# Performance work log

Hardware: AMD Instinct MI355X
Metric: run time of the kernel (lower is better)

## Reference

```python
import jax, jax.numpy as jnp
import numpy as np

B = 256
N_VERTS = 10475
N_JOINTS = 55  # 1 root + 21 body + jaw + 2 eyes + 2*15 hands
NUM_BETAS = 10
NUM_EXPR = 10
POSE_BASIS = (N_JOINTS - 1) * 9  # 486
# SMPL-X kinematic tree (parent index per joint, root = -1)
PARENTS = np.array([-1,0,0,0,1,2,3,4,5,6,7,8,9,9,9,12,13,14,16,17,18,19,15,15,15,
                    20,25,26,20,28,29,20,31,32,20,34,35,20,37,38,
                    21,40,41,21,43,44,21,46,47,21,49,50,21,52,53], dtype=np.int64)


def _rodrigues(aa):
    # axis-angle [..., 3] -> rotation matrix [..., 3, 3]
    angle = jnp.linalg.norm(aa, axis=-1, keepdims=True) + 1e-8
    axis = aa / angle
    x, y, z = axis[..., 0], axis[..., 1], axis[..., 2]
    zero = jnp.zeros_like(x)
    K = jnp.stack([zero, -z, y, z, zero, -x, -y, x, zero], axis=-1).reshape(aa.shape[:-1] + (3, 3))
    s = jnp.sin(angle)[..., None]
    c = jnp.cos(angle)[..., None]
    I = jnp.eye(3, dtype=aa.dtype)
    return I + s * K + (1.0 - c) * (K @ K)


def setup_inputs() -> dict:
    key = jax.random.key(0)
    ks = jax.random.split(key, 16)
    def rots(k, nj, scale=0.2):
        aa = jax.random.normal(k, (B, nj, 3), dtype=jnp.float32) * scale
        return _rodrigues(aa)
    inp = {
        'world_rot': rots(ks[0], 1, 0.5),
        'world_tsl': jax.random.normal(ks[1], (B, 3), dtype=jnp.float32),
        'body_shape': jax.random.normal(ks[2], (B, NUM_BETAS), dtype=jnp.float32),
        'body_pose': rots(ks[3], 21),
        'left_hand_pose': rots(ks[4], 15),
        'right_hand_pose': rots(ks[5], 15),
        'expr_shape': jax.random.normal(ks[6], (B, NUM_EXPR), dtype=jnp.float32),
        'jaw_pose': rots(ks[7], 1),
        'leye_pose': rots(ks[8], 1),
        'reye_pose': rots(ks[9], 1),
        # model buffers (synthetic, SMPL-X-sized)
        'v_template': jax.random.normal(ks[10], (N_VERTS, 3), dtype=jnp.float32) * 0.3,
        'shapedirs': jax.random.normal(ks[11], (N_VERTS, 3, NUM_BETAS), dtype=jnp.float32) * 0.01,
        'expr_dirs': jax.random.normal(ks[12], (N_VERTS, 3, NUM_EXPR), dtype=jnp.float32) * 0.01,
        'posedirs': jax.random.normal(ks[13], (POSE_BASIS, N_VERTS * 3), dtype=jnp.float32) * 0.01,
        'J_regressor': jax.nn.softmax(jax.random.normal(ks[14], (N_JOINTS, N_VERTS), dtype=jnp.float32) * 4.0, axis=-1),
        'lbs_weights': jax.nn.softmax(jax.random.normal(ks[15], (N_VERTS, N_JOINTS), dtype=jnp.float32) * 4.0, axis=-1),
    }
    return inp


def _lbs(world_rot, world_tsl, body_shape, body_pose, left_hand_pose, right_hand_pose,
         expr_shape, jaw_pose, leye_pose, reye_pose,
         v_template, shapedirs, expr_dirs, posedirs, J_regressor, lbs_weights):
    dtype = v_template.dtype
    # full pose: [B, 55, 3, 3]
    full_pose = jnp.concatenate([world_rot, body_pose, jaw_pose, leye_pose, reye_pose,
                                 left_hand_pose, right_hand_pose], axis=1)
    b = full_pose.shape[0]
    # shape + expression blendshapes
    v_shaped = v_template[None] + jnp.einsum('bk,nck->bnc', body_shape, shapedirs) \
               + jnp.einsum('bk,nck->bnc', expr_shape, expr_dirs)
    # rest-pose joints [B, J, 3]
    joints = jnp.einsum('jn,bnc->bjc', J_regressor, v_shaped)
    # pose blendshapes
    ident = jnp.eye(3, dtype=dtype)
    pose_feature = (full_pose[:, 1:] - ident).reshape(b, POSE_BASIS)
    v_posed = v_shaped + (pose_feature @ posedirs).reshape(b, N_VERTS, 3)
    # relative joint locations w.r.t. parent
    rel_joints = joints.at[:, 1:].add(-joints[:, PARENTS[1:]])
    # local 4x4 transforms [B, J, 4, 4]
    top = jnp.concatenate([full_pose, rel_joints[..., None]], axis=-1)  # [B,J,3,4]
    bottom = jnp.broadcast_to(jnp.array([0., 0., 0., 1.], dtype=dtype), (b, N_JOINTS, 1, 4))
    T = jnp.concatenate([top, bottom], axis=2)
    # kinematic chain recurrence (small fixed joint count -> unrolled)
    chain = [T[:, 0]]
    for i in range(1, N_JOINTS):
        chain.append(chain[PARENTS[i]] @ T[:, i])
    A = jnp.stack(chain, axis=1)  # [B, J, 4, 4]
    posed_joints = A[..., :3, 3]
    # remove rest-pose joint offset so A maps rest -> posed
    t_corr = posed_joints - jnp.einsum('bjkl,bjl->bjk', A[..., :3, :3], joints)
    A_rel = A.at[..., :3, 3].set(t_corr)
    # linear blend skinning: per-vertex transform [B, N, 4, 4]
    T_vert = jnp.einsum('nj,bjkl->bnkl', lbs_weights, A_rel)
    verts = jnp.einsum('bnkl,bnl->bnk', T_vert[..., :3, :3], v_posed) + T_vert[..., :3, 3]
    verts = verts + world_tsl[:, None]
    joints_out = posed_joints + world_tsl[:, None]
    return verts, joints_out


def reference(world_rot, world_tsl, body_shape, body_pose, left_hand_pose, right_hand_pose,
              expr_shape, jaw_pose, leye_pose, reye_pose,
              v_template, shapedirs, expr_dirs, posedirs, J_regressor, lbs_weights):
    return _lbs(world_rot, world_tsl, body_shape, body_pose, left_hand_pose, right_hand_pose,
                expr_shape, jaw_pose, leye_pose, reye_pose,
                v_template, shapedirs, expr_dirs, posedirs, J_regressor, lbs_weights)
```

## Files before the change

### kernel.cpp

```cpp
#include <hip/hip_runtime.h>
#include <stdint.h>

#define BATCH 256
#define NV 10475
#define NVP 10496
#define NJ 55
#define PB 486
#define KS 506
#define VC (NV*3)
#define KP 512
#define BKC 32
#define NCHUNK 16
#define BN 64
#define JCH 8
#define JCHUNK 1312

typedef short bf16x8 __attribute__((ext_vector_type(8)));
typedef float f32x4  __attribute__((ext_vector_type(4)));

__constant__ int c_parents[NJ] = {
  -1,0,0,0,1,2,3,4,5,6,7,8,9,9,9,12,13,14,16,17,18,19,15,15,15,
  20,25,26,20,28,29,20,31,32,20,34,35,20,37,38,21,40,41,21,43,44,
  21,46,47,21,49,50,21,52,53};

__constant__ int c_depth[NJ] = {
  0,1,1,1,2,2,2,3,3,3,4,4,4,4,4,5,5,5,6,6,7,7,6,6,6,
  8,9,10,8,9,10,8,9,10,8,9,10,8,9,10,
  8,9,10,8,9,10,8,9,10,8,9,10,8,9,10};

__device__ __forceinline__ unsigned short f2bf(float x){
  uint32_t u = __float_as_uint(x);
  uint32_t r = (u + 0x7fffu + ((u >> 16) & 1u)) >> 16;
  return (unsigned short)r;
}
__device__ __forceinline__ float bf2f(unsigned short h){
  return __uint_as_float(((uint32_t)h) << 16);
}

__global__ __launch_bounds__(256) void k_prep(
    const float* __restrict__ lw, unsigned short* __restrict__ lwb) {
  int idx = blockIdx.x*256 + threadIdx.x;
  int n = idx >> 6, j = idx & 63;
  float v = (n < NV && j < NJ) ? lw[(size_t)n*NJ + j] : 0.f;
  unsigned short hi = f2bf(v);
  float lo = v - bf2f(hi);
  lwb[idx] = hi;
  lwb[(size_t)NVP*64 + idx] = f2bf(lo);
}

__device__ __forceinline__ const float* pose_src(int j, int b,
    const float* wrot, const float* bpose, const float* jaw, const float* leye,
    const float* reye, const float* lhand, const float* rhand) {
  if (j==0)  return wrot  + b*9;
  if (j<=21) return bpose + (b*21 + (j-1))*9;
  if (j==22) return jaw   + b*9;
  if (j==23) return leye  + b*9;
  if (j==24) return reye  + b*9;
  if (j<=39) return lhand + (b*15 + (j-25))*9;
  return rhand + (b*15 + (j-40))*9;
}

__global__ __launch_bounds__(512) void k_posefeat(
    const float* __restrict__ bpose, const float* __restrict__ jaw,
    const float* __restrict__ leye, const float* __restrict__ reye,
    const float* __restrict__ lhand, const float* __restrict__ rhand,
    const float* __restrict__ bs, const float* __restrict__ es,
    unsigned short* __restrict__ pfb) {
  int b = blockIdx.x, t = threadIdx.x;
  unsigned short o = 0;
  if (t < PB){
    int jj = t/9, rc = t - jj*9;
    const float* rs = pose_src(jj+1, b, nullptr, bpose, jaw, leye, reye, lhand, rhand);
    float v = rs[rc];
    if (rc==0 || rc==4 || rc==8) v -= 1.0f;
    o = f2bf(v);
  } else if (t < 496){
    o = f2bf(bs[b*10 + (t-486)]);
  } else if (t < KS){
    o = f2bf(es[b*10 + (t-496)]);
  }
  pfb[(size_t)b*KP + t] = o;
}

__global__ __launch_bounds__(256) void k_jsmall(
    const float* __restrict__ jreg, const float* __restrict__ sd,
    const float* __restrict__ ed, const float* __restrict__ vt,
    float* __restrict__ part) {
  int ch = blockIdx.x, j = blockIdx.y;
  int t = threadIdx.x;
  float acc[63];
  #pragma unroll
  for (int s=0;s<63;s++) acc[s]=0.f;
  int n0 = ch*JCHUNK, nend = min(n0+JCHUNK, NV);
  for (int n = n0 + t; n < nend; n += 256){
    float w = jreg[(size_t)j*NV + n];
    const float* sp = sd + (size_t)n*30;
    const float* ep = ed + (size_t)n*30;
    const float* vp = vt + (size_t)n*3;
    #pragma unroll
    for (int c=0;c<3;c++){
      #pragma unroll
      for (int q=0;q<10;q++){
        acc[c*21+q]    += w*sp[c*10+q];
        acc[c*21+10+q] += w*ep[c*10+q];
      }
      acc[c*21+20] += w*vp[c];
    }
  }
  #pragma unroll
  for (int s=0;s<63;s++){
    float a = acc[s];
    #pragma unroll
    for (int d=32; d>=1; d>>=1) a += __shfl_xor(a,d);
    acc[s]=a;
  }
  __shared__ float red[4][63];
  int w = t>>6, l = t&63;
  if (l==0){
    #pragma unroll
    for (int s=0;s<63;s++) red[w][s]=acc[s];
  }
  __syncthreads();
  if (t < 63){
    float a = red[0][t]+red[1][t]+red[2][t]+red[3][t];
    part[((size_t)j*JCH+ch)*63 + t] = a;
  }
}

__global__ __launch_bounds__(192) void k_joints2(
    const float* __restrict__ part, const float* __restrict__ bs,
    const float* __restrict__ es, float* __restrict__ joints) {
  int b = blockIdx.x, t = threadIdx.x;
  if (t >= NJ*3) return;
  int j = t/3, c = t - j*3;
  float S[21];
  #pragma unroll
  for (int q=0;q<21;q++) S[q]=0.f;
  for (int ch=0; ch<JCH; ch++){
    const float* p = part + ((size_t)j*JCH+ch)*63 + c*21;
    #pragma unroll
    for (int q=0;q<21;q++) S[q] += p[q];
  }
  float a = S[20];
  #pragma unroll
  for (int q=0;q<10;q++) a += S[q]*bs[b*10+q] + S[10+q]*es[b*10+q];
  joints[(size_t)b*NJ*3 + t] = a;
}

__global__ __launch_bounds__(256) void k_chain(
    const float* __restrict__ wrot, const float* __restrict__ bpose,
    const float* __restrict__ jaw, const float* __restrict__ leye,
    const float* __restrict__ reye, const float* __restrict__ lhand,
    const float* __restrict__ rhand, const float* __restrict__ wtsl,
    const float* __restrict__ joints,
    unsigned short* __restrict__ arelb, float* __restrict__ jout) {
  const int w = threadIdx.x >> 6, lane = threadIdx.x & 63;
  const int b = blockIdx.x*4 + w;
  const int j = lane;
  const bool act = (j < NJ);

  float R[9] = {1.f,0.f,0.f, 0.f,1.f,0.f, 0.f,0.f,1.f};
  if (act){
    const float* rs = pose_src(j, b, wrot, bpose, jaw, leye, reye, lhand, rhand);
    #pragma unroll
    for (int i=0;i<9;i++) R[i]=rs[i];
  }
  float jx=0.f, jy=0.f, jz=0.f;
  if (act){
    const float* jb = joints + (size_t)b*NJ*3 + j*3;
    jx=jb[0]; jy=jb[1]; jz=jb[2];
  }
  int par = act ? c_parents[j] : 0;
  if (par < 0) par = 0;
  float px = __shfl(jx, par), py = __shfl(jy, par), pz = __shfl(jz, par);
  float t0, t1, t2;
  if (j == 0){ t0=jx; t1=jy; t2=jz; }
  else       { t0=jx-px; t1=jy-py; t2=jz-pz; }

  float M[12];
  #pragma unroll
  for (int r=0;r<3;r++){
    M[r*4+0]=R[r*3+0]; M[r*4+1]=R[r*3+1]; M[r*4+2]=R[r*3+2]; M[r*4+3]= (r==0?t0:(r==1?t1:t2));
  }
  int dep = act ? c_depth[j] : 99;

  #pragma unroll
  for (int L=1; L<=10; L++){
    float pm[12];
    #pragma unroll
    for (int i=0;i<12;i++) pm[i] = __shfl(M[i], par);
    if (dep == L){
      #pragma unroll
      for (int r=0;r<3;r++){
        float p0=pm[r*4+0], p1=pm[r*4+1], p2=pm[r*4+2], p3=pm[r*4+3];
        M[r*4+0] = p0*R[0]+p1*R[3]+p2*R[6];
        M[r*4+1] = p0*R[1]+p1*R[4]+p2*R[7];
        M[r*4+2] = p0*R[2]+p1*R[5]+p2*R[8];
        M[r*4+3] = p0*t0 + p1*t1 + p2*t2 + p3;
      }
    }
  }

  float wx=wtsl[b*3+0], wy=wtsl[b*3+1], wz=wtsl[b*3+2];
  if (act){
    jout[((size_t)b*NJ+j)*3+0] = M[3]  + wx;
    jout[((size_t)b*NJ+j)*3+1] = M[7]  + wy;
    jout[((size_t)b*NJ+j)*3+2] = M[11] + wz;
  }
  float A[12];
  #pragma unroll
  for (int r=0;r<3;r++){
    A[r*4+0]=M[r*4+0]; A[r*4+1]=M[r*4+1]; A[r*4+2]=M[r*4+2];
    A[r*4+3]=M[r*4+3] - (M[r*4+0]*jx + M[r*4+1]*jy + M[r*4+2]*jz);
  }
  unsigned short* ah = arelb + (size_t)(b*2+0)*16*64;
  unsigned short* al = arelb + (size_t)(b*2+1)*16*64;
  #pragma unroll
  for (int e=0;e<16;e++){
    float v = (e < 12 && act) ? A[e] : 0.f;
    unsigned short hi = f2bf(v);
    float lo = v - bf2f(hi);
    ah[e*64 + j] = hi;
    al[e*64 + j] = f2bf(lo);
  }
}

__global__ __launch_bounds__(256, 2) void k_vposed(
    const float* __restrict__ pd, const float* __restrict__ sd,
    const float* __restrict__ ed, const float* __restrict__ vt,
    const unsigned short* __restrict__ pfb, float* __restrict__ vsh) {
  const int tid  = threadIdx.x;
  const int w    = tid >> 6, lane = tid & 63;
  const int m16  = lane & 15, quad = lane >> 4;
  const int col0 = blockIdx.x * BN;

  f32x4 acc[4][4];
  #pragma unroll
  for (int i=0;i<4;i++)
    #pragma unroll
    for (int j=0;j<4;j++) acc[i][j] = (f32x4){0.f,0.f,0.f,0.f};

  int bcol[4];
  #pragma unroll
  for (int ni=0;ni<4;ni++) bcol[ni] = min(col0 + ni*16 + m16, VC-1);

  const unsigned short* pfa = pfb + (size_t)(w*64 + m16)*KP + quad*8;

  #pragma unroll 2
  for (int c=0; c<15; c++){
    const int k0 = c*BKC;
    bf16x8 a[4];
    #pragma unroll
    for (int mi=0;mi<4;mi++)
      a[mi] = *((const bf16x8*)(pfa + (size_t)mi*16*KP + k0));
    union { bf16x8 v; unsigned short s[8]; } bb[4];
    #pragma unroll
    for (int ni=0;ni<4;ni++){
      #pragma unroll
      for (int j=0;j<8;j++){
        int kk = k0 + quad*8 + j;
        bb[ni].s[j] = f2bf(pd[(size_t)kk*VC + bcol[ni]]);
      }
    }
    #pragma unroll
    for (int mi=0;mi<4;mi++)
      #pragma unroll
      for (int ni=0;ni<4;ni++)
        acc[mi][ni] = __builtin_amdgcn_mfma_f32_16x16x32_bf16(
                          a[mi], bb[ni].v, acc[mi][ni], 0, 0, 0);
  }
  {
    const int k0 = 15*BKC;
    bf16x8 a[4];
    #pragma unroll
    for (int mi=0;mi<4;mi++)
      a[mi] = *((const bf16x8*)(pfa + (size_t)mi*16*KP + k0));
    union { bf16x8 v; unsigned short s[8]; } bb[4];
    #pragma unroll
    for (int ni=0;ni<4;ni++){
      int n3 = bcol[ni]/3, c3 = bcol[ni] - n3*3;
      const float* sp = sd + (size_t)n3*30 + c3*10;
      const float* ep = ed + (size_t)n3*30 + c3*10;
      #pragma unroll
      for (int j=0;j<8;j++){
        int kk = k0 + quad*8 + j;
        float f = 0.f;
        if (kk < PB)      f = pd[(size_t)kk*VC + bcol[ni]];
        else if (kk < KS){
          int q = kk - PB;
          f = (q < 10) ? sp[q] : ep[q-10];
        }
        bb[ni].s[j] = f2bf(f);
      }
    }
    #pragma unroll
    for (int mi=0;mi<4;mi++)
      #pragma unroll
      for (int ni=0;ni<4;ni++)
        acc[mi][ni] = __builtin_amdgcn_mfma_f32_16x16x32_bf16(
                          a[mi], bb[ni].v, acc[mi][ni], 0, 0, 0);
  }
  #pragma unroll
  for (int mi=0;mi<4;mi++){
    int rbase = w*64 + mi*16 + quad*4;
    #pragma unroll
    for (int ni=0;ni<4;ni++){
      int col = col0 + ni*16 + m16;
      if (col < VC){
        float vtc = vt[col];
        #pragma unroll
        for (int r=0;r<4;r++)
          vsh[(size_t)(rbase + r)*VC + col] = acc[mi][ni][r] + vtc;
      }
    }
  }
}

__global__ __launch_bounds__(256) void k_verts(
    const unsigned short* __restrict__ lwb, const unsigned short* __restrict__ arelb,
    const float* __restrict__ wtsl, float* __restrict__ out) {
  __shared__ float sT[4*64*17];
  const int tid = threadIdx.x, w = tid >> 6, lane = tid & 63;
  const int m16 = lane & 15, quad = lane >> 4;
  const int n0 = blockIdx.x*64;
  const int b0 = blockIdx.y*16;
  float* myT = &sT[w*64*17];

  bf16x8 lwh[4][2], lwl[4][2];
  #pragma unroll
  for (int vt4=0; vt4<4; vt4++){
    int row = n0 + vt4*16 + m16;
    #pragma unroll
    for (int kc=0;kc<2;kc++){
      lwh[vt4][kc] = *((const bf16x8*)(lwb + (size_t)row*64 + kc*32 + quad*8));
      lwl[vt4][kc] = *((const bf16x8*)(lwb + (size_t)NVP*64 + (size_t)row*64 + kc*32 + quad*8));
    }
  }
  const int nA = n0 + lane;
  const bool okA = (nA < NV);

  for (int bi=0; bi<4; bi++){
    const int b = b0 + w*4 + bi;
    bf16x8 ah[2], al[2];
    #pragma unroll
    for (int kc=0;kc<2;kc++){
      ah[kc] = *((const bf16x8*)(arelb + ((size_t)(b*2+0)*16 + m16)*64 + kc*32 + quad*8));
      al[kc] = *((const bf16x8*)(arelb + ((size_t)(b*2+1)*16 + m16)*64 + kc*32 + quad*8));
    }
    const float* vp = out + ((size_t)b*NV + nA)*3;
    float vx = okA ? vp[0] : 0.f;
    float vy = okA ? vp[1] : 0.f;
    float vz = okA ? vp[2] : 0.f;

    f32x4 acc[4];
    #pragma unroll
    for (int vt4=0; vt4<4; vt4++) acc[vt4] = (f32x4){0.f,0.f,0.f,0.f};
    #pragma unroll
    for (int vt4=0; vt4<4; vt4++){
      #pragma unroll
      for (int kc=0;kc<2;kc++){
        acc[vt4] = __builtin_amdgcn_mfma_f32_16x16x32_bf16(ah[kc], lwh[vt4][kc], acc[vt4], 0,0,0);
        acc[vt4] = __builtin_amdgcn_mfma_f32_16x16x32_bf16(al[kc], lwh[vt4][kc], acc[vt4], 0,0,0);
        acc[vt4] = __builtin_amdgcn_mfma_f32_16x16x32_bf16(ah[kc], lwl[vt4][kc], acc[vt4], 0,0,0);
      }
    }
    #pragma unroll
    for (int vt4=0; vt4<4; vt4++){
      #pragma unroll
      for (int r=0;r<4;r++)
        myT[(vt4*16 + m16)*17 + quad*4 + r] = acc[vt4][r];
    }
    float T[12];
    const float* Tp = &myT[lane*17];
    #pragma unroll
    for (int e=0;e<12;e++) T[e] = Tp[e];
    if (okA){
      float tx=wtsl[b*3+0], ty=wtsl[b*3+1], tz=wtsl[b*3+2];
      float* op = out + ((size_t)b*NV + nA)*3;
      op[0] = T[0]*vx + T[1]*vy + T[2] *vz + T[3]  + tx;
      op[1] = T[4]*vx + T[5]*vy + T[6] *vz + T[7]  + ty;
      op[2] = T[8]*vx + T[9]*vy + T[10]*vz + T[11] + tz;
    }
  }
}

extern "C" void kernel_launch(void* const* d_in, const int* in_sizes, int n_in,
                              void* d_out, int out_size, void* d_ws, size_t ws_size,
                              hipStream_t stream) {
  const float* wrot   = (const float*)d_in[0];
  const float* wtsl   = (const float*)d_in[1];
  const float* bshape = (const float*)d_in[2];
  const float* bpose  = (const float*)d_in[3];
  const float* lhand  = (const float*)d_in[4];
  const float* rhand  = (const float*)d_in[5];
  const float* eshape = (const float*)d_in[6];
  const float* jaw    = (const float*)d_in[7];
  const float* leye   = (const float*)d_in[8];
  const float* reye   = (const float*)d_in[9];
  const float* vt     = (const float*)d_in[10];
  const float* sd     = (const float*)d_in[11];
  const float* ed     = (const float*)d_in[12];
  const float* pd     = (const float*)d_in[13];
  const float* jreg   = (const float*)d_in[14];
  const float* lw     = (const float*)d_in[15];
  float* out = (float*)d_out;

  float* vsh  = out;
  float* jout = out + (size_t)BATCH*NV*3;

  float* ws     = (float*)d_ws;
  float* joints = ws;
  float* part   = joints + (size_t)BATCH*NJ*3;
  unsigned short* pfb   = (unsigned short*)(part + (size_t)NJ*JCH*63);
  unsigned short* lwb   = pfb + (size_t)BATCH*KP;
  unsigned short* arelb = lwb + (size_t)2*NVP*64;

  const int PREP_BLOCKS = (NVP*64)/256;

  k_prep    <<<PREP_BLOCKS, 256, 0, stream>>>(lw, lwb);
  k_posefeat<<<BATCH, 512, 0, stream>>>(bpose, jaw, leye, reye, lhand, rhand,
                                        bshape, eshape, pfb);
  k_jsmall  <<<dim3(JCH, NJ), 256, 0, stream>>>(jreg, sd, ed, vt, part);
  k_joints2 <<<BATCH, 192, 0, stream>>>(part, bshape, eshape, joints);
  k_chain   <<<64, 256, 0, stream>>>(wrot, bpose, jaw, leye, reye, lhand, rhand,
                                     wtsl, joints, arelb, jout);
  k_vposed  <<<(VC+BN-1)/BN, 256, 0, stream>>>(pd, sd, ed, vt, pfb, vsh);
  k_verts   <<<dim3(NVP/64, 16), 256, 0, stream>>>(lwb, arelb, wtsl, out);
}
```

Measured before the change: 246.9 us.

## Pre-pack posedirs to bf16 MFMA layout and widen vposed blocks

Adds a prep stage that converts posedirs plus the shape and expression dirs into a padded bf16 buffer laid out in MFMA B-fragment order. The vposed GEMM then does one vector load per fragment instead of eight strided fp32 loads with conversions. It also moves to 512-thread blocks with 2 M-tiles per wave. Separately, k_verts stores transforms in shared memory with a transposed stride-68 layout to cut bank conflicts. The cost is an extra pass over posedirs every call to write the roughly 32MB packed copy.

```diff
diff --git a/kernel.cpp b/kernel.cpp
--- a/kernel.cpp
+++ b/kernel.cpp
@@ -8,6 +8,7 @@
 #define PB 486
 #define KS 506
 #define VC (NV*3)
+#define VCP 31488
 #define KP 512
 #define BKC 32
 #define NCHUNK 16
@@ -38,14 +39,47 @@
 }
 
 __global__ __launch_bounds__(256) void k_prep(
-    const float* __restrict__ lw, unsigned short* __restrict__ lwb) {
-  int idx = blockIdx.x*256 + threadIdx.x;
-  int n = idx >> 6, j = idx & 63;
-  float v = (n < NV && j < NJ) ? lw[(size_t)n*NJ + j] : 0.f;
-  unsigned short hi = f2bf(v);
-  float lo = v - bf2f(hi);
-  lwb[idx] = hi;
-  lwb[(size_t)NVP*64 + idx] = f2bf(lo);
+    const float* __restrict__ lw, const float* __restrict__ pd,
+    const float* __restrict__ sd, const float* __restrict__ ed,
+    unsigned short* __restrict__ lwb, unsigned short* __restrict__ pdb) {
+  int bid = blockIdx.x;
+  const int LWB_BLOCKS = (NVP*64)/256;
+  if (bid < LWB_BLOCKS) {
+    int idx = bid*256 + threadIdx.x;
+    int n = idx >> 6, j = idx & 63;
+    float v = (n < NV && j < NJ) ? lw[(size_t)n*NJ + j] : 0.f;
+    unsigned short hi = f2bf(v);
+    float lo = v - bf2f(hi);
+    lwb[idx] = hi;
+    lwb[(size_t)NVP*64 + idx] = f2bf(lo);
+  } else {
+    int idx = (bid - LWB_BLOCKS)*256 + threadIdx.x;
+    int c   = idx / (VCP*4);
+    int rem = idx - c*(VCP*4);
+    int col = rem >> 2, q = rem & 3;
+    int kb  = c*32 + q*8;
+    union { bf16x8 v; unsigned short s[8]; } u;
+    if (col < VC){
+      int n3 = col/3, c3 = col - n3*3;
+      const float* sp = sd + (size_t)n3*30 + c3*10;
+      const float* ep = ed + (size_t)n3*30 + c3*10;
+      #pragma unroll
+      for (int j=0;j<8;j++){
+        int k = kb + j;
+        float f = 0.f;
+        if (k < PB)      f = pd[(size_t)k*VC + col];
+        else if (k < KS){
+          int qq = k - PB;
+          f = (qq < 10) ? sp[qq] : ep[qq-10];
+        }
+        u.s[j] = f2bf(f);
+      }
+    } else {
+      #pragma unroll
+      for (int j=0;j<8;j++) u.s[j] = 0;
+    }
+    *((bf16x8*)(pdb + (size_t)idx*8)) = u.v;
+  }
 }
 
 __device__ __forceinline__ const float* pose_src(int j, int b,
@@ -225,84 +259,44 @@
   }
 }
 
-__global__ __launch_bounds__(256, 2) void k_vposed(
-    const float* __restrict__ pd, const float* __restrict__ sd,
-    const float* __restrict__ ed, const float* __restrict__ vt,
+__global__ __launch_bounds__(512) void k_vposed(
+    const unsigned short* __restrict__ pdb, const float* __restrict__ vt,
     const unsigned short* __restrict__ pfb, float* __restrict__ vsh) {
   const int tid  = threadIdx.x;
   const int w    = tid >> 6, lane = tid & 63;
   const int m16  = lane & 15, quad = lane >> 4;
   const int col0 = blockIdx.x * BN;
 
-  f32x4 acc[4][4];
-  #pragma unroll
-  for (int i=0;i<4;i++)
+  f32x4 acc[2][4];
+  #pragma unroll
+  for (int i=0;i<2;i++)
     #pragma unroll
     for (int j=0;j<4;j++) acc[i][j] = (f32x4){0.f,0.f,0.f,0.f};
 
-  int bcol[4];
-  #pragma unroll
-  for (int ni=0;ni<4;ni++) bcol[ni] = min(col0 + ni*16 + m16, VC-1);
-
-  const unsigned short* pfa = pfb + (size_t)(w*64 + m16)*KP + quad*8;
+  const unsigned short* pfa = pfb + (size_t)(w*32 + m16)*KP + quad*8;
 
   #pragma unroll 2
-  for (int c=0; c<15; c++){
-    const int k0 = c*BKC;
-    bf16x8 a[4];
-    #pragma unroll
-    for (int mi=0;mi<4;mi++)
-      a[mi] = *((const bf16x8*)(pfa + (size_t)mi*16*KP + k0));
-    union { bf16x8 v; unsigned short s[8]; } bb[4];
+  for (int c=0; c<NCHUNK; c++){
+    bf16x8 a[2];
+    #pragma unroll
+    for (int mi=0;mi<2;mi++)
+      a[mi] = *((const bf16x8*)(pfa + (size_t)mi*16*KP + c*BKC));
+    bf16x8 bq[4];
     #pragma unroll
     for (int ni=0;ni<4;ni++){
-      #pragma unroll
-      for (int j=0;j<8;j++){
-        int kk = k0 + quad*8 + j;
-        bb[ni].s[j] = f2bf(pd[(size_t)kk*VC + bcol[ni]]);
-      }
-    }
-    #pragma unroll
-    for (int mi=0;mi<4;mi++)
+      size_t g = ((size_t)c*VCP + (col0 + ni*16 + m16))*4 + quad;
+      bq[ni] = *((const bf16x8*)(pdb + g*8));
+    }
+    #pragma unroll
+    for (int mi=0;mi<2;mi++)
       #pragma unroll
       for (int ni=0;ni<4;ni++)
         acc[mi][ni] = __builtin_amdgcn_mfma_f32_16x16x32_bf16(
-                          a[mi], bb[ni].v, acc[mi][ni], 0, 0, 0);
-  }
-  {
-    const int k0 = 15*BKC;
-    bf16x8 a[4];
-    #pragma unroll
-    for (int mi=0;mi<4;mi++)
-      a[mi] = *((const bf16x8*)(pfa + (size_t)mi*16*KP + k0));
-    union { bf16x8 v; unsigned short s[8]; } bb[4];
-    #pragma unroll
-    for (int ni=0;ni<4;ni++){
-      int n3 = bcol[ni]/3, c3 = bcol[ni] - n3*3;
-      const float* sp = sd + (size_t)n3*30 + c3*10;
-      const float* ep = ed + (size_t)n3*30 + c3*10;
-      #pragma unroll
-      for (int j=0;j<8;j++){
-        int kk = k0 + quad*8 + j;
-        float f = 0.f;
-        if (kk < PB)      f = pd[(size_t)kk*VC + bcol[ni]];
-        else if (kk < KS){
-          int q = kk - PB;
-          f = (q < 10) ? sp[q] : ep[q-10];
-        }
-        bb[ni].s[j] = f2bf(f);
-      }
-    }
-    #pragma unroll
-    for (int mi=0;mi<4;mi++)
-      #pragma unroll
-      for (int ni=0;ni<4;ni++)
-        acc[mi][ni] = __builtin_amdgcn_mfma_f32_16x16x32_bf16(
-                          a[mi], bb[ni].v, acc[mi][ni], 0, 0, 0);
-  }
-  #pragma unroll
-  for (int mi=0;mi<4;mi++){
-    int rbase = w*64 + mi*16 + quad*4;
+                          a[mi], bq[ni], acc[mi][ni], 0, 0, 0);
+  }
+  #pragma unroll
+  for (int mi=0;mi<2;mi++){
+    int rbase = w*32 + mi*16 + quad*4;
     #pragma unroll
     for (int ni=0;ni<4;ni++){
       int col = col0 + ni*16 + m16;
@@ -319,12 +313,12 @@
 __global__ __launch_bounds__(256) void k_verts(
     const unsigned short* __restrict__ lwb, const unsigned short* __restrict__ arelb,
     const float* __restrict__ wtsl, float* __restrict__ out) {
-  __shared__ float sT[4*64*17];
+  __shared__ float sT[4*816];
   const int tid = threadIdx.x, w = tid >> 6, lane = tid & 63;
   const int m16 = lane & 15, quad = lane >> 4;
   const int n0 = blockIdx.x*64;
   const int b0 = blockIdx.y*16;
-  float* myT = &sT[w*64*17];
+  float* myT = &sT[w*816];
 
   bf16x8 lwh[4][2], lwl[4][2];
   #pragma unroll
@@ -366,14 +360,15 @@
     }
     #pragma unroll
     for (int vt4=0; vt4<4; vt4++){
-      #pragma unroll
-      for (int r=0;r<4;r++)
-        myT[(vt4*16 + m16)*17 + quad*4 + r] = acc[vt4][r];
+      if (quad < 3){
+        #pragma unroll
+        for (int r=0;r<4;r++)
+          myT[(quad*4 + r)*68 + vt4*16 + m16] = acc[vt4][r];
+      }
     }
     float T[12];
-    const float* Tp = &myT[lane*17];
-    #pragma unroll
-    for (int e=0;e<12;e++) T[e] = Tp[e];
+    #pragma unroll
+    for (int e=0;e<12;e++) T[e] = myT[e*68 + lane];
     if (okA){
       float tx=wtsl[b*3+0], ty=wtsl[b*3+1], tz=wtsl[b*3+2];
       float* op = out + ((size_t)b*NV + nA)*3;
@@ -414,16 +409,17 @@
   unsigned short* pfb   = (unsigned short*)(part + (size_t)NJ*JCH*63);
   unsigned short* lwb   = pfb + (size_t)BATCH*KP;
   unsigned short* arelb = lwb + (size_t)2*NVP*64;
-
-  const int PREP_BLOCKS = (NVP*64)/256;
-
-  k_prep    <<<PREP_BLOCKS, 256, 0, stream>>>(lw, lwb);
+  unsigned short* pdb   = arelb + (size_t)BATCH*2*16*64;
+
+  const int LWB_BLOCKS = (NVP*64)/256;
+  const int PDB_BLOCKS = (NCHUNK*VCP*4)/256;
+  k_prep    <<<LWB_BLOCKS + PDB_BLOCKS, 256, 0, stream>>>(lw, pd, sd, ed, lwb, pdb);
   k_posefeat<<<BATCH, 512, 0, stream>>>(bpose, jaw, leye, reye, lhand, rhand,
                                         bshape, eshape, pfb);
   k_jsmall  <<<dim3(JCH, NJ), 256, 0, stream>>>(jreg, sd, ed, vt, part);
   k_joints2 <<<BATCH, 192, 0, stream>>>(part, bshape, eshape, joints);
   k_chain   <<<64, 256, 0, stream>>>(wrot, bpose, jaw, leye, reye, lhand, rhand,
                                      wtsl, joints, arelb, jout);
-  k_vposed  <<<(VC+BN-1)/BN, 256, 0, stream>>>(pd, sd, ed, vt, pfb, vsh);
+  k_vposed  <<<(VC+BN-1)/BN, 512, 0, stream>>>(pdb, vt, pfb, vsh);
   k_verts   <<<dim3(NVP/64, 16), 256, 0, stream>>>(lwb, arelb, wtsl, out);
 }
```

Result: slower. 261.9 us (+6.1%).

## Merge prep kernels into one launch and fuse joint regression with chain

Applied to the files above, without the earlier changes.

The lbs-weight bf16 split, pose-feature packing and joint-regressor partial sums now run as three block ranges of a single front kernel. Joint assembly and the kinematic chain are fused into one per-batch kernel that passes joints through shared memory. The k_verts shared transpose also switches to a row-per-element layout so the quad-3 lanes skip their stores. Together these cut seven launches to four and drop the joints round-trip through global memory. In exchange, k_mid runs one batch per 256-thread block with only 64 threads active in the chain phase.

```diff
diff --git a/kernel.cpp b/kernel.cpp
--- a/kernel.cpp
+++ b/kernel.cpp
@@ -37,17 +37,6 @@
   return __uint_as_float(((uint32_t)h) << 16);
 }
 
-__global__ __launch_bounds__(256) void k_prep(
-    const float* __restrict__ lw, unsigned short* __restrict__ lwb) {
-  int idx = blockIdx.x*256 + threadIdx.x;
-  int n = idx >> 6, j = idx & 63;
-  float v = (n < NV && j < NJ) ? lw[(size_t)n*NJ + j] : 0.f;
-  unsigned short hi = f2bf(v);
-  float lo = v - bf2f(hi);
-  lwb[idx] = hi;
-  lwb[(size_t)NVP*64 + idx] = f2bf(lo);
-}
-
 __device__ __forceinline__ const float* pose_src(int j, int b,
     const float* wrot, const float* bpose, const float* jaw, const float* leye,
     const float* reye, const float* lhand, const float* rhand) {
@@ -60,103 +49,120 @@
   return rhand + (b*15 + (j-40))*9;
 }
 
-__global__ __launch_bounds__(512) void k_posefeat(
+#define LWB_BLOCKS 2624
+#define PF_BLOCKS  BATCH
+#define JS_BLOCKS  (JCH*NJ)
+#define FRONT_BLOCKS (LWB_BLOCKS + PF_BLOCKS + JS_BLOCKS)
+
+__global__ __launch_bounds__(256) void k_front(
+    const float* __restrict__ lw,
     const float* __restrict__ bpose, const float* __restrict__ jaw,
     const float* __restrict__ leye, const float* __restrict__ reye,
     const float* __restrict__ lhand, const float* __restrict__ rhand,
     const float* __restrict__ bs, const float* __restrict__ es,
-    unsigned short* __restrict__ pfb) {
-  int b = blockIdx.x, t = threadIdx.x;
-  unsigned short o = 0;
-  if (t < PB){
-    int jj = t/9, rc = t - jj*9;
-    const float* rs = pose_src(jj+1, b, nullptr, bpose, jaw, leye, reye, lhand, rhand);
-    float v = rs[rc];
-    if (rc==0 || rc==4 || rc==8) v -= 1.0f;
-    o = f2bf(v);
-  } else if (t < 496){
-    o = f2bf(bs[b*10 + (t-486)]);
-  } else if (t < KS){
-    o = f2bf(es[b*10 + (t-496)]);
-  }
-  pfb[(size_t)b*KP + t] = o;
-}
-
-__global__ __launch_bounds__(256) void k_jsmall(
     const float* __restrict__ jreg, const float* __restrict__ sd,
     const float* __restrict__ ed, const float* __restrict__ vt,
+    unsigned short* __restrict__ lwb, unsigned short* __restrict__ pfb,
     float* __restrict__ part) {
-  int ch = blockIdx.x, j = blockIdx.y;
-  int t = threadIdx.x;
-  float acc[63];
-  #pragma unroll
-  for (int s=0;s<63;s++) acc[s]=0.f;
-  int n0 = ch*JCHUNK, nend = min(n0+JCHUNK, NV);
-  for (int n = n0 + t; n < nend; n += 256){
-    float w = jreg[(size_t)j*NV + n];
-    const float* sp = sd + (size_t)n*30;
-    const float* ep = ed + (size_t)n*30;
-    const float* vp = vt + (size_t)n*3;
-    #pragma unroll
-    for (int c=0;c<3;c++){
-      #pragma unroll
-      for (int q=0;q<10;q++){
-        acc[c*21+q]    += w*sp[c*10+q];
-        acc[c*21+10+q] += w*ep[c*10+q];
-      }
-      acc[c*21+20] += w*vp[c];
-    }
-  }
-  #pragma unroll
-  for (int s=0;s<63;s++){
-    float a = acc[s];
-    #pragma unroll
-    for (int d=32; d>=1; d>>=1) a += __shfl_xor(a,d);
-    acc[s]=a;
-  }
-  __shared__ float red[4][63];
-  int w = t>>6, l = t&63;
-  if (l==0){
-    #pragma unroll
-    for (int s=0;s<63;s++) red[w][s]=acc[s];
-  }
-  __syncthreads();
-  if (t < 63){
-    float a = red[0][t]+red[1][t]+red[2][t]+red[3][t];
-    part[((size_t)j*JCH+ch)*63 + t] = a;
-  }
-}
-
-__global__ __launch_bounds__(192) void k_joints2(
+  const int bid = blockIdx.x, t = threadIdx.x;
+  if (bid < LWB_BLOCKS) {
+    int idx = bid*256 + t;
+    int n = idx >> 6, j = idx & 63;
+    float v = (n < NV && j < NJ) ? lw[(size_t)n*NJ + j] : 0.f;
+    unsigned short hi = f2bf(v);
+    float lo = v - bf2f(hi);
+    lwb[idx] = hi;
+    lwb[(size_t)NVP*64 + idx] = f2bf(lo);
+  } else if (bid < LWB_BLOCKS + PF_BLOCKS) {
+    int b = bid - LWB_BLOCKS;
+    #pragma unroll
+    for (int half=0; half<2; half++){
+      int tt = t + half*256;
+      unsigned short o = 0;
+      if (tt < PB){
+        int jj = tt/9, rc = tt - jj*9;
+        const float* rs = pose_src(jj+1, b, nullptr, bpose, jaw, leye, reye, lhand, rhand);
+        float v = rs[rc];
+        if (rc==0 || rc==4 || rc==8) v -= 1.0f;
+        o = f2bf(v);
+      } else if (tt < 496){
+        o = f2bf(bs[b*10 + (tt-486)]);
+      } else if (tt < KS){
+        o = f2bf(es[b*10 + (tt-496)]);
+      }
+      pfb[(size_t)b*KP + tt] = o;
+    }
+  } else {
+    int idx = bid - (LWB_BLOCKS + PF_BLOCKS);
+    int ch = idx & 7, j = idx >> 3;
+    float acc[63];
+    #pragma unroll
+    for (int s=0;s<63;s++) acc[s]=0.f;
+    int n0 = ch*JCHUNK, nend = min(n0+JCHUNK, NV);
+    for (int n = n0 + t; n < nend; n += 256){
+      float w = jreg[(size_t)j*NV + n];
+      const float* sp = sd + (size_t)n*30;
+      const float* ep = ed + (size_t)n*30;
+      const float* vp = vt + (size_t)n*3;
+      #pragma unroll
+      for (int c=0;c<3;c++){
+        #pragma unroll
+        for (int q=0;q<10;q++){
+          acc[c*21+q]    += w*sp[c*10+q];
+          acc[c*21+10+q] += w*ep[c*10+q];
+        }
+        acc[c*21+20] += w*vp[c];
+      }
+    }
+    #pragma unroll
+    for (int s=0;s<63;s++){
+      float a = acc[s];
+      #pragma unroll
+      for (int d=32; d>=1; d>>=1) a += __shfl_xor(a,d);
+      acc[s]=a;
+    }
+    __shared__ float red[4][63];
+    int w = t>>6, l = t&63;
+    if (l==0){
+      #pragma unroll
+      for (int s=0;s<63;s++) red[w][s]=acc[s];
+    }
+    __syncthreads();
+    if (t < 63){
+      float a = red[0][t]+red[1][t]+red[2][t]+red[3][t];
+      part[((size_t)j*JCH+ch)*63 + t] = a;
+    }
+  }
+}
+
+__global__ __launch_bounds__(256) void k_mid(
     const float* __restrict__ part, const float* __restrict__ bs,
-    const float* __restrict__ es, float* __restrict__ joints) {
-  int b = blockIdx.x, t = threadIdx.x;
-  if (t >= NJ*3) return;
-  int j = t/3, c = t - j*3;
-  float S[21];
-  #pragma unroll
-  for (int q=0;q<21;q++) S[q]=0.f;
-  for (int ch=0; ch<JCH; ch++){
-    const float* p = part + ((size_t)j*JCH+ch)*63 + c*21;
-    #pragma unroll
-    for (int q=0;q<21;q++) S[q] += p[q];
-  }
-  float a = S[20];
-  #pragma unroll
-  for (int q=0;q<10;q++) a += S[q]*bs[b*10+q] + S[10+q]*es[b*10+q];
-  joints[(size_t)b*NJ*3 + t] = a;
-}
-
-__global__ __launch_bounds__(256) void k_chain(
+    const float* __restrict__ es,
     const float* __restrict__ wrot, const float* __restrict__ bpose,
     const float* __restrict__ jaw, const float* __restrict__ leye,
     const float* __restrict__ reye, const float* __restrict__ lhand,
     const float* __restrict__ rhand, const float* __restrict__ wtsl,
-    const float* __restrict__ joints,
     unsigned short* __restrict__ arelb, float* __restrict__ jout) {
-  const int w = threadIdx.x >> 6, lane = threadIdx.x & 63;
-  const int b = blockIdx.x*4 + w;
-  const int j = lane;
+  __shared__ float jlds[NJ*3];
+  const int b = blockIdx.x, t = threadIdx.x;
+  if (t < NJ*3){
+    int j = t/3, c = t - j*3;
+    float S[21];
+    #pragma unroll
+    for (int q=0;q<21;q++) S[q]=0.f;
+    for (int ch=0; ch<JCH; ch++){
+      const float* p = part + ((size_t)j*JCH+ch)*63 + c*21;
+      #pragma unroll
+      for (int q=0;q<21;q++) S[q] += p[q];
+    }
+    float a = S[20];
+    #pragma unroll
+    for (int q=0;q<10;q++) a += S[q]*bs[b*10+q] + S[10+q]*es[b*10+q];
+    jlds[t] = a;
+  }
+  __syncthreads();
+  if (t >= 64) return;
+  const int j = t;
   const bool act = (j < NJ);
 
   float R[9] = {1.f,0.f,0.f, 0.f,1.f,0.f, 0.f,0.f,1.f};
@@ -166,10 +172,7 @@
     for (int i=0;i<9;i++) R[i]=rs[i];
   }
   float jx=0.f, jy=0.f, jz=0.f;
-  if (act){
-    const float* jb = joints + (size_t)b*NJ*3 + j*3;
-    jx=jb[0]; jy=jb[1]; jz=jb[2];
-  }
+  if (act){ jx=jlds[j*3+0]; jy=jlds[j*3+1]; jz=jlds[j*3+2]; }
   int par = act ? c_parents[j] : 0;
   if (par < 0) par = 0;
   float px = __shfl(jx, par), py = __shfl(jy, par), pz = __shfl(jz, par);
@@ -319,12 +322,12 @@
 __global__ __launch_bounds__(256) void k_verts(
     const unsigned short* __restrict__ lwb, const unsigned short* __restrict__ arelb,
     const float* __restrict__ wtsl, float* __restrict__ out) {
-  __shared__ float sT[4*64*17];
+  __shared__ float sT[4*816];
   const int tid = threadIdx.x, w = tid >> 6, lane = tid & 63;
   const int m16 = lane & 15, quad = lane >> 4;
   const int n0 = blockIdx.x*64;
   const int b0 = blockIdx.y*16;
-  float* myT = &sT[w*64*17];
+  float* myT = &sT[w*816];
 
   bf16x8 lwh[4][2], lwl[4][2];
   #pragma unroll
@@ -366,14 +369,15 @@
     }
     #pragma unroll
     for (int vt4=0; vt4<4; vt4++){
-      #pragma unroll
-      for (int r=0;r<4;r++)
-        myT[(vt4*16 + m16)*17 + quad*4 + r] = acc[vt4][r];
+      if (quad < 3){
+        #pragma unroll
+        for (int r=0;r<4;r++)
+          myT[(quad*4 + r)*68 + vt4*16 + m16] = acc[vt4][r];
+      }
     }
     float T[12];
-    const float* Tp = &myT[lane*17];
-    #pragma unroll
-    for (int e=0;e<12;e++) T[e] = Tp[e];
+    #pragma unroll
+    for (int e=0;e<12;e++) T[e] = myT[e*68 + lane];
     if (okA){
       float tx=wtsl[b*3+0], ty=wtsl[b*3+1], tz=wtsl[b*3+2];
       float* op = out + ((size_t)b*NV + nA)*3;
@@ -408,22 +412,17 @@
   float* vsh  = out;
   float* jout = out + (size_t)BATCH*NV*3;
 
-  float* ws     = (float*)d_ws;
-  float* joints = ws;
-  float* part   = joints + (size_t)BATCH*NJ*3;
+  float* ws   = (float*)d_ws;
+  float* part = ws;
   unsigned short* pfb   = (unsigned short*)(part + (size_t)NJ*JCH*63);
   unsigned short* lwb   = pfb + (size_t)BATCH*KP;
   unsigned short* arelb = lwb + (size_t)2*NVP*64;
 
-  const int PREP_BLOCKS = (NVP*64)/256;
-
-  k_prep    <<<PREP_BLOCKS, 256, 0, stream>>>(lw, lwb);
-  k_posefeat<<<BATCH, 512, 0, stream>>>(bpose, jaw, leye, reye, lhand, rhand,
-                                        bshape, eshape, pfb);
-  k_jsmall  <<<dim3(JCH, NJ), 256, 0, stream>>>(jreg, sd, ed, vt, part);
-  k_joints2 <<<BATCH, 192, 0, stream>>>(part, bshape, eshape, joints);
-  k_chain   <<<64, 256, 0, stream>>>(wrot, bpose, jaw, leye, reye, lhand, rhand,
-                                     wtsl, joints, arelb, jout);
-  k_vposed  <<<(VC+BN-1)/BN, 256, 0, stream>>>(pd, sd, ed, vt, pfb, vsh);
-  k_verts   <<<dim3(NVP/64, 16), 256, 0, stream>>>(lwb, arelb, wtsl, out);
-}
+  k_front <<<FRONT_BLOCKS, 256, 0, stream>>>(lw, bpose, jaw, leye, reye,
+                                             lhand, rhand, bshape, eshape,
+                                             jreg, sd, ed, vt, lwb, pfb, part);
+  k_mid   <<<BATCH, 256, 0, stream>>>(part, bshape, eshape, wrot, bpose, jaw,
+                                      leye, reye, lhand, rhand, wtsl, arelb, jout);
+  k_vposed<<<(VC+BN-1)/BN, 256, 0, stream>>>(pd, sd, ed, vt, pfb, vsh);
+  k_verts <<<dim3(NVP/64, 16), 256, 0, stream>>>(lwb, arelb, wtsl, out);
+}
```

New measurement: 246.8 us. About the same (-0.0%).
